# Kernel optimization log

Hardware: AMD Instinct MI355X
Metric: run time of the kernel (lower is better)

## Reference

```python
import jax, jax.numpy as jnp
import numpy as np

IN_CH = 1024
EMB = 1024
OUT = 768


def setup_inputs() -> dict:
    key = jax.random.key(0)
    ks = jax.random.split(key, 12)
    B, S = 8, 2048
    std = 1.0 / np.sqrt(IN_CH)
    return {
        "image_embeds": jax.random.normal(ks[0], (B, S, IN_CH), jnp.float32),
        "ref_pose_embeds": jax.random.normal(ks[1], (B, S, IN_CH), jnp.float32),
        "pose_embeds": jax.random.normal(ks[2], (B, S, IN_CH), jnp.float32),
        "ln_gamma": jnp.ones((IN_CH,), jnp.float32),
        "ln_beta": jnp.zeros((IN_CH,), jnp.float32),
        "Wq": jax.random.normal(ks[3], (EMB, IN_CH), jnp.float32) * std,
        "bq": jnp.zeros((EMB,), jnp.float32),
        "Wk": jax.random.normal(ks[4], (EMB, IN_CH), jnp.float32) * std,
        "bk": jnp.zeros((EMB,), jnp.float32),
        "Wv": jax.random.normal(ks[5], (EMB, IN_CH), jnp.float32) * std,
        "bv": jnp.zeros((EMB,), jnp.float32),
        "Wo": jax.random.normal(ks[6], (OUT, EMB), jnp.float32) * (1.0 / np.sqrt(EMB)),
        "bo": jnp.zeros((OUT,), jnp.float32),
    }


def _layernorm(x, gamma, beta, eps=1e-5):
    mu = jnp.mean(x, axis=-1, keepdims=True)
    var = jnp.var(x, axis=-1, keepdims=True)
    return (x - mu) * jax.lax.rsqrt(var + eps) * gamma + beta


def reference(image_embeds, ref_pose_embeds, pose_embeds,
              ln_gamma, ln_beta, Wq, bq, Wk, bk, Wv, bv, Wo, bo):
    scale = EMB ** (-0.5)
    # shared LayerNorm applied to all three streams (as in original)
    img_n = _layernorm(image_embeds, ln_gamma, ln_beta)
    ref_n = _layernorm(ref_pose_embeds, ln_gamma, ln_beta)
    pose_n = _layernorm(pose_embeds, ln_gamma, ln_beta)
    Q = ref_n @ Wq.T + bq   # [B,S,E]
    K = pose_n @ Wk.T + bk
    V = img_n @ Wv.T + bv
    att = jnp.einsum('bid,bjd->bij', Q, K) * scale  # [B,S,S]
    att = jax.nn.softmax(att, axis=-1)
    out = jnp.einsum('bij,bjd->bid', att, V)
    out = out + pose_n + img_n
    return out @ Wo.T + bo  # [B,S,768]
```

## Files before the change

kernel.cpp:

```cpp
#include <hip/hip_runtime.h>
#include <hip/hip_bf16.h>
#include <hip/hip_fp16.h>

typedef __attribute__((ext_vector_type(8))) short short8;
typedef __attribute__((ext_vector_type(4))) float f32x4;
typedef unsigned short u16;

__device__ __forceinline__ u16 f2bf(float f) {
  union { float f; unsigned u; } v; v.f = f;
  unsigned r = v.u + 0x7fffu + ((v.u >> 16) & 1u);
  return (u16)(r >> 16);
}
__device__ __forceinline__ float bf2f(u16 u) {
  union { unsigned u; float f; } v; v.u = ((unsigned)u) << 16;
  return v.f;
}
__device__ __forceinline__ void gload16(const void* g, void* l) {
  __builtin_amdgcn_global_load_lds(
      (const __attribute__((address_space(1))) unsigned*)g,
      (__attribute__((address_space(3))) unsigned*)l, 16, 0, 0);
}

#define FENCE asm volatile("" ::: "memory")

__global__ __launch_bounds__(256)
void ln_bf16(const float* __restrict__ X, const float* __restrict__ gamma,
             const float* __restrict__ beta, u16* __restrict__ Y) {
  const int row = blockIdx.x;
  const int tid = threadIdx.x;
  const long base = (long)row * 1024 + tid * 4;
  float4 x = *(const float4*)(X + base);
  float s = x.x + x.y + x.z + x.w;
  float q = x.x * x.x + x.y * x.y + x.z * x.z + x.w * x.w;
#pragma unroll
  for (int o = 32; o > 0; o >>= 1) {
    s += __shfl_xor(s, o);
    q += __shfl_xor(q, o);
  }
  __shared__ float rs[4], rq[4];
  if ((tid & 63) == 0) { rs[tid >> 6] = s; rq[tid >> 6] = q; }
  __syncthreads();
  s = rs[0] + rs[1] + rs[2] + rs[3];
  q = rq[0] + rq[1] + rq[2] + rq[3];
  float mu = s * (1.f / 1024.f);
  float var = q * (1.f / 1024.f) - mu * mu;
  float rstd = rsqrtf(var + 1e-5f);
  float4 g = *(const float4*)(gamma + tid * 4);
  float4 b = *(const float4*)(beta + tid * 4);
  ushort4 o4;
  o4.x = f2bf((x.x - mu) * rstd * g.x + b.x);
  o4.y = f2bf((x.y - mu) * rstd * g.y + b.y);
  o4.z = f2bf((x.z - mu) * rstd * g.z + b.z);
  o4.w = f2bf((x.w - mu) * rstd * g.w + b.w);
  *(ushort4*)(Y + base) = o4;
}

__global__ __launch_bounds__(256)
void cvt_bf16(const float* __restrict__ in, u16* __restrict__ out, int n4) {
  int i = blockIdx.x * blockDim.x + threadIdx.x;
  if (i < n4) {
    float4 x = ((const float4*)in)[i];
    ushort4 o;
    o.x = f2bf(x.x); o.y = f2bf(x.y); o.z = f2bf(x.z); o.w = f2bf(x.w);
    ((ushort4*)out)[i] = o;
  }
}

__global__ __launch_bounds__(256)
void softmax_inplace(u16* __restrict__ LP) {
  const int tid = threadIdx.x;
  const long base = (long)blockIdx.x * 2048 + tid * 8;
  const __half* hp = (const __half*)LP + base;
  short8 raw = *(const short8*)hp;
  float x[8];
#pragma unroll
  for (int i = 0; i < 8; ++i) x[i] = __half2float(((const __half*)&raw)[i]);
  float m = x[0];
#pragma unroll
  for (int i = 1; i < 8; ++i) m = fmaxf(m, x[i]);
#pragma unroll
  for (int o = 32; o > 0; o >>= 1) m = fmaxf(m, __shfl_xor(m, o));
  __shared__ float red[8];
  if ((tid & 63) == 0) red[tid >> 6] = m;
  __syncthreads();
  m = fmaxf(fmaxf(red[0], red[1]), fmaxf(red[2], red[3]));
  float e[8];
  float s = 0.f;
#pragma unroll
  for (int i = 0; i < 8; ++i) { e[i] = __expf(x[i] - m); s += e[i]; }
#pragma unroll
  for (int o = 32; o > 0; o >>= 1) s += __shfl_xor(s, o);
  if ((tid & 63) == 0) red[4 + (tid >> 6)] = s;
  __syncthreads();
  s = red[4] + red[5] + red[6] + red[7];
  float inv = 1.f / s;
  short8 out;
#pragma unroll
  for (int i = 0; i < 8; ++i) ((u16*)&out)[i] = f2bf(e[i] * inv);
  *(short8*)((__half*)LP + base) = out;
}

template <int MODE>
__global__ __launch_bounds__(512, 2)
void gemm256(const u16* __restrict__ A, const u16* __restrict__ B,
             const float* __restrict__ bias, void* __restrict__ Cp,
             const u16* __restrict__ R1, const u16* __restrict__ R2,
             int M, int N, int K, long sA, long sB, long sC, float scale) {
  extern __shared__ char lds[];
  const int bz = blockIdx.z;
  const u16* Ab = A + (long)bz * sA;
  const u16* Bb = B + (long)bz * sB;
  const long cb = (long)bz * sC;

  const int tid = threadIdx.x;
  const int lane = tid & 63;
  const int wid = tid >> 6;
  const int wr = wid >> 2;
  const int wc = wid & 3;
  const long rowBase = (long)blockIdx.y * 256;
  const long colBase = (long)blockIdx.x * 256;
  const int fr = lane & 15;
  const int fk = lane >> 4;
  const int nt = K >> 6;

  auto stage = [&](const u16* __restrict__ gb, long rcBase, int t, int h, int bOff) {
    char* base = lds + (t & 1) * 65536 + bOff + h * 16384;
    const long kk = (long)t << 6;
#pragma unroll
    for (int i = 0; i < 2; ++i) {
      const int o = i * 8192 + tid * 16;
      const int row = o >> 7;
      const int cs = (o >> 4) & 7;
      const long gr = rcBase + h * 128 + row;
      const long gk = kk + (long)((cs ^ (row & 7)) << 3);
      gload16(gb + gr * (long)K + gk, base + o);
    }
  };

  auto ldA = [&](int t, int m, int ks) -> short8 {
    const int row = wr * 128 + m * 16 + fr;
    const int ch = (ks * 4 + fk) ^ (row & 7);
    return *(const short8*)(lds + (t & 1) * 65536 + row * 128 + ch * 16);
  };
  auto ldB = [&](int t, int n, int ks) -> short8 {
    const int row = wc * 64 + n * 16 + fr;
    const int ch = (ks * 4 + fk) ^ (row & 7);
    return *(const short8*)(lds + (t & 1) * 65536 + 32768 + row * 128 + ch * 16);
  };

  f32x4 acc[8][4] = {};
  short8 bq[4][2];

  stage(Ab, rowBase, 0, 0, 0);
  stage(Ab, rowBase, 0, 1, 0);
  stage(Bb, colBase, 0, 0, 32768);
  stage(Bb, colBase, 0, 1, 32768);
  if (nt > 1) {
    stage(Ab, rowBase, 1, 0, 0);
    stage(Bb, colBase, 1, 0, 32768);
    stage(Bb, colBase, 1, 1, 32768);
    asm volatile("s_waitcnt vmcnt(6)" ::: "memory");
  } else {
    asm volatile("s_waitcnt vmcnt(0)" ::: "memory");
  }
  FENCE; __builtin_amdgcn_s_barrier(); FENCE;

#define DO_PHASE(M0, STAGE, VMW)                                                                         \
  do {                                                                                                   \
    short8 a00 = ldA(t, (M0), 0), a01 = ldA(t, (M0), 1);                                                 \
    short8 a10 = ldA(t, (M0) + 1, 0), a11 = ldA(t, (M0) + 1, 1);                                         \
    STAGE;                                                                                               \
    VMW;                                                                                                 \
    FENCE; __builtin_amdgcn_s_barrier(); FENCE;                                                          \
    __builtin_amdgcn_s_setprio(1);                                                                       \
    _Pragma("unroll")                                                                                    \
    for (int n = 0; n < 4; ++n) {                                                                        \
      acc[(M0)][n] = __builtin_amdgcn_mfma_f32_16x16x32_bf16(a00, bq[n][0], acc[(M0)][n], 0, 0, 0);      \
      acc[(M0)][n] = __builtin_amdgcn_mfma_f32_16x16x32_bf16(a01, bq[n][1], acc[(M0)][n], 0, 0, 0);      \
      acc[(M0) + 1][n] = __builtin_amdgcn_mfma_f32_16x16x32_bf16(a10, bq[n][0], acc[(M0) + 1][n], 0, 0, 0); \
      acc[(M0) + 1][n] = __builtin_amdgcn_mfma_f32_16x16x32_bf16(a11, bq[n][1], acc[(M0) + 1][n], 0, 0, 0); \
    }                                                                                                    \
    __builtin_amdgcn_s_setprio(0);                                                                       \
    FENCE; __builtin_amdgcn_s_barrier(); FENCE;                                                          \
  } while (0)

  for (int t = 0; t < nt; ++t) {
#pragma unroll
    for (int n = 0; n < 4; ++n) {
      bq[n][0] = ldB(t, n, 0);
      bq[n][1] = ldB(t, n, 1);
    }
    DO_PHASE(0, { if (t + 1 < nt) stage(Ab, rowBase, t + 1, 1, 0); }, {});
    DO_PHASE(2, { if (t + 2 < nt) stage(Bb, colBase, t + 2, 0, 32768); }, {});
    DO_PHASE(4, { if (t + 2 < nt) stage(Bb, colBase, t + 2, 1, 32768); }, {});
    DO_PHASE(6, { if (t + 2 < nt) stage(Ab, rowBase, t + 2, 0, 0); },
             {
               if (t + 2 < nt) { asm volatile("s_waitcnt vmcnt(6)" ::: "memory"); }
               else            { asm volatile("s_waitcnt vmcnt(0)" ::: "memory"); }
             });
  }
#undef DO_PHASE

#pragma unroll
  for (int m = 0; m < 8; ++m) {
#pragma unroll
    for (int n = 0; n < 4; ++n) {
#pragma unroll
      for (int j = 0; j < 4; ++j) {
        long r = rowBase + wr * 128 + m * 16 + fk * 4 + j;
        long c = colBase + wc * 64 + n * 16 + fr;
        float v = acc[m][n][j];
        if (MODE == 0) {
          ((u16*)Cp)[cb + r * N + c] = f2bf(v + bias[c]);
        } else if (MODE == 1) {
          ((__half*)Cp)[cb + r * N + c] = __float2half(v * scale);
        } else if (MODE == 2) {
          long b2 = r >> 11;
          long i = r & 2047;
          ((u16*)Cp)[b2 * (1024L * 2048) + c * 2048 + i] = f2bf(v + bias[c]);
        } else if (MODE == 3) {
          long idx = cb + r * N + c;
          ((u16*)Cp)[idx] = f2bf(v + bf2f(R1[idx]) + bf2f(R2[idx]));
        } else {
          ((float*)Cp)[cb + r * N + c] = v + bias[c];
        }
      }
    }
  }
}

extern "C" void kernel_launch(void* const* d_in, const int* in_sizes, int n_in,
                              void* d_out, int out_size, void* d_ws, size_t ws_size,
                              hipStream_t stream) {
  const float* img  = (const float*)d_in[0];
  const float* refp = (const float*)d_in[1];
  const float* pose = (const float*)d_in[2];
  const float* gam  = (const float*)d_in[3];
  const float* bet  = (const float*)d_in[4];
  const float* Wq = (const float*)d_in[5];
  const float* bq = (const float*)d_in[6];
  const float* Wk = (const float*)d_in[7];
  const float* bk = (const float*)d_in[8];
  const float* Wv = (const float*)d_in[9];
  const float* bv = (const float*)d_in[10];
  const float* Wo = (const float*)d_in[11];
  const float* bo = (const float*)d_in[12];

  char* ws = (char*)d_ws;
  const size_t MB = 1u << 20;
  u16* Wq_b = (u16*)(ws + 0 * MB);
  u16* Wk_b = (u16*)(ws + 2 * MB);
  u16* Wv_b = (u16*)(ws + 4 * MB);
  u16* Wo_b = (u16*)(ws + 6 * MB);
  u16* bufA = (u16*)(ws + 8 * MB);
  u16* bufB = (u16*)(ws + 40 * MB);
  u16* bufC = (u16*)(ws + 72 * MB);
  u16* bufD = (u16*)(ws + 104 * MB);
  u16* bufE = (u16*)(ws + 136 * MB);
  u16* bufL = (u16*)(ws + 168 * MB);

  const int LDSB = 131072;
  hipFuncSetAttribute((const void*)gemm256<0>, hipFuncAttributeMaxDynamicSharedMemorySize, LDSB);
  hipFuncSetAttribute((const void*)gemm256<1>, hipFuncAttributeMaxDynamicSharedMemorySize, LDSB);
  hipFuncSetAttribute((const void*)gemm256<2>, hipFuncAttributeMaxDynamicSharedMemorySize, LDSB);
  hipFuncSetAttribute((const void*)gemm256<3>, hipFuncAttributeMaxDynamicSharedMemorySize, LDSB);
  hipFuncSetAttribute((const void*)gemm256<4>, hipFuncAttributeMaxDynamicSharedMemorySize, LDSB);

  cvt_bf16<<<1024, 256, 0, stream>>>(Wq, Wq_b, 1024 * 1024 / 4);
  cvt_bf16<<<1024, 256, 0, stream>>>(Wk, Wk_b, 1024 * 1024 / 4);
  cvt_bf16<<<1024, 256, 0, stream>>>(Wv, Wv_b, 1024 * 1024 / 4);
  cvt_bf16<<<768, 256, 0, stream>>>(Wo, Wo_b, 768 * 1024 / 4);

  ln_bf16<<<16384, 256, 0, stream>>>(refp, gam, bet, bufA);
  ln_bf16<<<16384, 256, 0, stream>>>(pose, gam, bet, bufB);
  ln_bf16<<<16384, 256, 0, stream>>>(img, gam, bet, bufC);

  gemm256<0><<<dim3(4, 64, 1), 512, LDSB, stream>>>(bufA, Wq_b, bq, bufD, nullptr, nullptr,
                                                    16384, 1024, 1024, 0, 0, 0, 1.f);
  gemm256<2><<<dim3(4, 64, 1), 512, LDSB, stream>>>(bufC, Wv_b, bv, bufE, nullptr, nullptr,
                                                    16384, 1024, 1024, 0, 0, 0, 1.f);
  gemm256<0><<<dim3(4, 64, 1), 512, LDSB, stream>>>(bufB, Wk_b, bk, bufA, nullptr, nullptr,
                                                    16384, 1024, 1024, 0, 0, 0, 1.f);
  gemm256<1><<<dim3(8, 8, 8), 512, LDSB, stream>>>(bufD, bufA, nullptr, bufL, nullptr, nullptr,
                                                   2048, 2048, 1024,
                                                   2048L * 1024, 2048L * 1024, 2048L * 2048,
                                                   0.03125f);
  softmax_inplace<<<16384, 256, 0, stream>>>(bufL);
  gemm256<3><<<dim3(4, 8, 8), 512, LDSB, stream>>>(bufL, bufE, nullptr, bufD, bufB, bufC,
                                                   2048, 1024, 2048,
                                                   2048L * 2048, 1024L * 2048, 2048L * 1024, 1.f);
  gemm256<4><<<dim3(3, 64, 1), 512, LDSB, stream>>>(bufD, Wo_b, bo, d_out, nullptr, nullptr,
                                                    16384, 768, 1024, 0, 0, 0, 1.f);
}
```

Before: 400.6 us.

## Restructure GEMM main loop into 4x2 MFMA blocks, swap operands for vectorized epilogue

```diff
diff --git a/kernel.cpp b/kernel.cpp
--- a/kernel.cpp
+++ b/kernel.cpp
@@ -15,6 +15,11 @@
   union { unsigned u; float f; } v; v.u = ((unsigned)u) << 16;
   return v.f;
 }
+__device__ __forceinline__ u16 f2h(float f) {
+  __half h = __float2half(f);
+  union { __half h; u16 u; } v; v.h = h;
+  return v.u;
+}
 __device__ __forceinline__ void gload16(const void* g, void* l) {
   __builtin_amdgcn_global_load_lds(
       (const __attribute__((address_space(1))) unsigned*)g,
@@ -22,12 +27,17 @@
 }
 
 #define FENCE asm volatile("" ::: "memory")
+#define SB0 __builtin_amdgcn_sched_barrier(0)
 
 __global__ __launch_bounds__(256)
-void ln_bf16(const float* __restrict__ X, const float* __restrict__ gamma,
-             const float* __restrict__ beta, u16* __restrict__ Y) {
+void ln3(const float* __restrict__ refp, const float* __restrict__ pose,
+         const float* __restrict__ img, const float* __restrict__ gamma,
+         const float* __restrict__ beta, u16* __restrict__ oA,
+         u16* __restrict__ oB, u16* __restrict__ oC) {
   const int row = blockIdx.x;
   const int tid = threadIdx.x;
+  const float* X = (blockIdx.y == 0) ? refp : (blockIdx.y == 1) ? pose : img;
+  u16* Y = (blockIdx.y == 0) ? oA : (blockIdx.y == 1) ? oB : oC;
   const long base = (long)row * 1024 + tid * 4;
   float4 x = *(const float4*)(X + base);
   float s = x.x + x.y + x.z + x.w;
@@ -56,14 +66,23 @@
 }
 
 __global__ __launch_bounds__(256)
-void cvt_bf16(const float* __restrict__ in, u16* __restrict__ out, int n4) {
-  int i = blockIdx.x * blockDim.x + threadIdx.x;
-  if (i < n4) {
-    float4 x = ((const float4*)in)[i];
-    ushort4 o;
-    o.x = f2bf(x.x); o.y = f2bf(x.y); o.z = f2bf(x.z); o.w = f2bf(x.w);
-    ((ushort4*)out)[i] = o;
-  }
+void cvt_all(const float* __restrict__ Wq, const float* __restrict__ Wk,
+             const float* __restrict__ Wv, const float* __restrict__ Wo,
+             u16* __restrict__ oq, u16* __restrict__ ok, u16* __restrict__ ov,
+             u16* __restrict__ oo) {
+  int i = blockIdx.x * 256 + threadIdx.x;
+  const int W1 = 262144;
+  const float* src;
+  u16* dst;
+  int j;
+  if (i < W1) { src = Wq; dst = oq; j = i; }
+  else if (i < 2 * W1) { src = Wk; dst = ok; j = i - W1; }
+  else if (i < 3 * W1) { src = Wv; dst = ov; j = i - 2 * W1; }
+  else { src = Wo; dst = oo; j = i - 3 * W1; }
+  float4 x = ((const float4*)src)[j];
+  ushort4 o;
+  o.x = f2bf(x.x); o.y = f2bf(x.y); o.z = f2bf(x.z); o.w = f2bf(x.w);
+  ((ushort4*)dst)[j] = o;
 }
 
 __global__ __launch_bounds__(256)
@@ -149,7 +168,8 @@
   };
 
   f32x4 acc[8][4] = {};
-  short8 bq[4][2];
+  short8 ar[4][2];
+  short8 br[4][2];
 
   stage(Ab, rowBase, 0, 0, 0);
   stage(Ab, rowBase, 0, 1, 0);
@@ -165,65 +185,92 @@
   }
   FENCE; __builtin_amdgcn_s_barrier(); FENCE;
 
-#define DO_PHASE(M0, STAGE, VMW)                                                                         \
-  do {                                                                                                   \
-    short8 a00 = ldA(t, (M0), 0), a01 = ldA(t, (M0), 1);                                                 \
-    short8 a10 = ldA(t, (M0) + 1, 0), a11 = ldA(t, (M0) + 1, 1);                                         \
-    STAGE;                                                                                               \
-    VMW;                                                                                                 \
-    FENCE; __builtin_amdgcn_s_barrier(); FENCE;                                                          \
-    __builtin_amdgcn_s_setprio(1);                                                                       \
-    _Pragma("unroll")                                                                                    \
-    for (int n = 0; n < 4; ++n) {                                                                        \
-      acc[(M0)][n] = __builtin_amdgcn_mfma_f32_16x16x32_bf16(a00, bq[n][0], acc[(M0)][n], 0, 0, 0);      \
-      acc[(M0)][n] = __builtin_amdgcn_mfma_f32_16x16x32_bf16(a01, bq[n][1], acc[(M0)][n], 0, 0, 0);      \
-      acc[(M0) + 1][n] = __builtin_amdgcn_mfma_f32_16x16x32_bf16(a10, bq[n][0], acc[(M0) + 1][n], 0, 0, 0); \
-      acc[(M0) + 1][n] = __builtin_amdgcn_mfma_f32_16x16x32_bf16(a11, bq[n][1], acc[(M0) + 1][n], 0, 0, 0); \
-    }                                                                                                    \
-    __builtin_amdgcn_s_setprio(0);                                                                       \
-    FENCE; __builtin_amdgcn_s_barrier(); FENCE;                                                          \
-  } while (0)
+#define MFMA16(MB, NB)                                                               \
+  __builtin_amdgcn_s_setprio(1);                                                     \
+  _Pragma("unroll") for (int k2 = 0; k2 < 2; ++k2)                                   \
+  _Pragma("unroll") for (int nn = 0; nn < 2; ++nn)                                   \
+  _Pragma("unroll") for (int mm = 0; mm < 4; ++mm)                                   \
+      acc[(MB) + mm][(NB) + nn] = __builtin_amdgcn_mfma_f32_16x16x32_bf16(           \
+          ar[mm][k2], br[(NB) + nn][k2], acc[(MB) + mm][(NB) + nn], 0, 0, 0);        \
+  __builtin_amdgcn_s_setprio(0);
 
   for (int t = 0; t < nt; ++t) {
 #pragma unroll
+    for (int mm = 0; mm < 4; ++mm) { ar[mm][0] = ldA(t, mm, 0); ar[mm][1] = ldA(t, mm, 1); }
+#pragma unroll
+    for (int nn = 0; nn < 2; ++nn) { br[nn][0] = ldB(t, nn, 0); br[nn][1] = ldB(t, nn, 1); }
+    if (t + 1 < nt) stage(Ab, rowBase, t + 1, 1, 0);
+    FENCE; __builtin_amdgcn_s_barrier(); FENCE; SB0;
+    MFMA16(0, 0);
+    SB0; FENCE; __builtin_amdgcn_s_barrier(); FENCE;
+
+#pragma unroll
+    for (int nn = 2; nn < 4; ++nn) { br[nn][0] = ldB(t, nn, 0); br[nn][1] = ldB(t, nn, 1); }
+    FENCE; __builtin_amdgcn_s_barrier(); FENCE; SB0;
+    MFMA16(0, 2);
+    SB0; FENCE; __builtin_amdgcn_s_barrier(); FENCE;
+
+#pragma unroll
+    for (int mm = 0; mm < 4; ++mm) { ar[mm][0] = ldA(t, 4 + mm, 0); ar[mm][1] = ldA(t, 4 + mm, 1); }
+    if (t + 2 < nt) stage(Bb, colBase, t + 2, 0, 32768);
+    FENCE; __builtin_amdgcn_s_barrier(); FENCE; SB0;
+    MFMA16(4, 0);
+    SB0; FENCE; __builtin_amdgcn_s_barrier(); FENCE;
+
+    if (t + 2 < nt) {
+      stage(Bb, colBase, t + 2, 1, 32768);
+      stage(Ab, rowBase, t + 2, 0, 0);
+      asm volatile("s_waitcnt vmcnt(6)" ::: "memory");
+    } else {
+      asm volatile("s_waitcnt vmcnt(0)" ::: "memory");
+    }
+    FENCE; __builtin_amdgcn_s_barrier(); FENCE; SB0;
+    MFMA16(4, 2);
+    SB0; FENCE; __builtin_amdgcn_s_barrier(); FENCE;
+  }
+#undef MFMA16
+
+#pragma unroll
+  for (int m = 0; m < 8; ++m) {
+#pragma unroll
     for (int n = 0; n < 4; ++n) {
-      bq[n][0] = ldB(t, n, 0);
-      bq[n][1] = ldB(t, n, 1);
-    }
-    DO_PHASE(0, { if (t + 1 < nt) stage(Ab, rowBase, t + 1, 1, 0); }, {});
-    DO_PHASE(2, { if (t + 2 < nt) stage(Bb, colBase, t + 2, 0, 32768); }, {});
-    DO_PHASE(4, { if (t + 2 < nt) stage(Bb, colBase, t + 2, 1, 32768); }, {});
-    DO_PHASE(6, { if (t + 2 < nt) stage(Ab, rowBase, t + 2, 0, 0); },
-             {
-               if (t + 2 < nt) { asm volatile("s_waitcnt vmcnt(6)" ::: "memory"); }
-               else            { asm volatile("s_waitcnt vmcnt(0)" ::: "memory"); }
-             });
-  }
-#undef DO_PHASE
-
-#pragma unroll
-  for (int m = 0; m < 8; ++m) {
-#pragma unroll
-    for (int n = 0; n < 4; ++n) {
-#pragma unroll
-      for (int j = 0; j < 4; ++j) {
-        long r = rowBase + wr * 128 + m * 16 + fk * 4 + j;
-        long c = colBase + wc * 64 + n * 16 + fr;
-        float v = acc[m][n][j];
-        if (MODE == 0) {
-          ((u16*)Cp)[cb + r * N + c] = f2bf(v + bias[c]);
-        } else if (MODE == 1) {
-          ((__half*)Cp)[cb + r * N + c] = __float2half(v * scale);
-        } else if (MODE == 2) {
-          long b2 = r >> 11;
-          long i = r & 2047;
-          ((u16*)Cp)[b2 * (1024L * 2048) + c * 2048 + i] = f2bf(v + bias[c]);
-        } else if (MODE == 3) {
-          long idx = cb + r * N + c;
-          ((u16*)Cp)[idx] = f2bf(v + bf2f(R1[idx]) + bf2f(R2[idx]));
-        } else {
-          ((float*)Cp)[cb + r * N + c] = v + bias[c];
-        }
+      const long r = rowBase + wr * 128 + m * 16 + fk * 4;
+      const long c = colBase + wc * 64 + n * 16 + fr;
+      f32x4 v = acc[m][n];
+      if (MODE == 0) {
+        float4 bb = *(const float4*)(bias + r);
+        ushort4 o;
+        o.x = f2bf(v[0] + bb.x); o.y = f2bf(v[1] + bb.y);
+        o.z = f2bf(v[2] + bb.z); o.w = f2bf(v[3] + bb.w);
+        *(ushort4*)((u16*)Cp + c * (long)M + r) = o;
+      } else if (MODE == 1) {
+        ushort4 o;
+        o.x = f2h(v[0] * scale); o.y = f2h(v[1] * scale);
+        o.z = f2h(v[2] * scale); o.w = f2h(v[3] * scale);
+        *(ushort4*)((u16*)Cp + cb + c * (long)M + r) = o;
+      } else if (MODE == 2) {
+        const long b2 = r >> 11;
+        const long i = r & 2047;
+        const float bc = bias[c];
+        ushort4 o;
+        o.x = f2bf(v[0] + bc); o.y = f2bf(v[1] + bc);
+        o.z = f2bf(v[2] + bc); o.w = f2bf(v[3] + bc);
+        *(ushort4*)((u16*)Cp + b2 * 2097152L + c * 2048L + i) = o;
+      } else if (MODE == 3) {
+        const long idx = cb + c * (long)M + r;
+        ushort4 r1 = *(const ushort4*)(R1 + idx);
+        ushort4 r2 = *(const ushort4*)(R2 + idx);
+        ushort4 o;
+        o.x = f2bf(v[0] + bf2f(r1.x) + bf2f(r2.x));
+        o.y = f2bf(v[1] + bf2f(r1.y) + bf2f(r2.y));
+        o.z = f2bf(v[2] + bf2f(r1.z) + bf2f(r2.z));
+        o.w = f2bf(v[3] + bf2f(r1.w) + bf2f(r2.w));
+        *(ushort4*)((u16*)Cp + idx) = o;
+      } else {
+        float4 bb = *(const float4*)(bias + r);
+        float4 o;
+        o.x = v[0] + bb.x; o.y = v[1] + bb.y; o.z = v[2] + bb.z; o.w = v[3] + bb.w;
+        *(float4*)((float*)Cp + c * (long)M + r) = o;
       }
     }
   }
@@ -266,29 +313,24 @@
   hipFuncSetAttribute((const void*)gemm256<3>, hipFuncAttributeMaxDynamicSharedMemorySize, LDSB);
   hipFuncSetAttribute((const void*)gemm256<4>, hipFuncAttributeMaxDynamicSharedMemorySize, LDSB);
 
-  cvt_bf16<<<1024, 256, 0, stream>>>(Wq, Wq_b, 1024 * 1024 / 4);
-  cvt_bf16<<<1024, 256, 0, stream>>>(Wk, Wk_b, 1024 * 1024 / 4);
-  cvt_bf16<<<1024, 256, 0, stream>>>(Wv, Wv_b, 1024 * 1024 / 4);
-  cvt_bf16<<<768, 256, 0, stream>>>(Wo, Wo_b, 768 * 1024 / 4);
-
-  ln_bf16<<<16384, 256, 0, stream>>>(refp, gam, bet, bufA);
-  ln_bf16<<<16384, 256, 0, stream>>>(pose, gam, bet, bufB);
-  ln_bf16<<<16384, 256, 0, stream>>>(img, gam, bet, bufC);
-
-  gemm256<0><<<dim3(4, 64, 1), 512, LDSB, stream>>>(bufA, Wq_b, bq, bufD, nullptr, nullptr,
-                                                    16384, 1024, 1024, 0, 0, 0, 1.f);
+  cvt_all<<<3840, 256, 0, stream>>>(Wq, Wk, Wv, Wo, Wq_b, Wk_b, Wv_b, Wo_b);
+
+  ln3<<<dim3(16384, 3), 256, 0, stream>>>(refp, pose, img, gam, bet, bufA, bufB, bufC);
+
+  gemm256<0><<<dim3(64, 4, 1), 512, LDSB, stream>>>(Wq_b, bufA, bq, bufD, nullptr, nullptr,
+                                                    1024, 16384, 1024, 0, 0, 0, 1.f);
+  gemm256<0><<<dim3(64, 4, 1), 512, LDSB, stream>>>(Wk_b, bufB, bk, bufA, nullptr, nullptr,
+                                                    1024, 16384, 1024, 0, 0, 0, 1.f);
   gemm256<2><<<dim3(4, 64, 1), 512, LDSB, stream>>>(bufC, Wv_b, bv, bufE, nullptr, nullptr,
                                                     16384, 1024, 1024, 0, 0, 0, 1.f);
-  gemm256<0><<<dim3(4, 64, 1), 512, LDSB, stream>>>(bufB, Wk_b, bk, bufA, nullptr, nullptr,
-                                                    16384, 1024, 1024, 0, 0, 0, 1.f);
-  gemm256<1><<<dim3(8, 8, 8), 512, LDSB, stream>>>(bufD, bufA, nullptr, bufL, nullptr, nullptr,
+  gemm256<1><<<dim3(8, 8, 8), 512, LDSB, stream>>>(bufA, bufD, nullptr, bufL, nullptr, nullptr,
                                                    2048, 2048, 1024,
                                                    2048L * 1024, 2048L * 1024, 2048L * 2048,
                                                    0.03125f);
   softmax_inplace<<<16384, 256, 0, stream>>>(bufL);
-  gemm256<3><<<dim3(4, 8, 8), 512, LDSB, stream>>>(bufL, bufE, nullptr, bufD, bufB, bufC,
-                                                   2048, 1024, 2048,
-                                                   2048L * 2048, 1024L * 2048, 2048L * 1024, 1.f);
-  gemm256<4><<<dim3(3, 64, 1), 512, LDSB, stream>>>(bufD, Wo_b, bo, d_out, nullptr, nullptr,
-                                                    16384, 768, 1024, 0, 0, 0, 1.f);
-}
+  gemm256<3><<<dim3(8, 4, 8), 512, LDSB, stream>>>(bufE, bufL, nullptr, bufD, bufB, bufC,
+                                                   1024, 2048, 2048,
+                                                   1024L * 2048, 2048L * 2048, 2048L * 1024, 1.f);
+  gemm256<4><<<dim3(64, 3, 1), 512, LDSB, stream>>>(Wo_b, bufD, bo, d_out, nullptr, nullptr,
+                                                    768, 16384, 1024, 0, 0, 0, 1.f);
+}
```

Result: slower. 417.3 us (+4.2%).
